# Kernel optimization log

Measured on AMD Instinct MI355X. Metric: run time of the kernel, lower is better.

## Reference

```python
import jax, jax.numpy as jnp
import numpy as np

EMBED_DIM = 1024
NUM_HEADS = 16
PROJ_DIM = EMBED_DIM // NUM_HEADS


def setup_inputs() -> dict:
    key = jax.random.key(0)
    ks = jax.random.split(key, 11)
    B, S, D = 2, 2048, EMBED_DIM
    scale = 1.0 / np.sqrt(D)
    inp = {
        'q': jax.random.normal(ks[0], (B, S, D), jnp.float32),
        'k': jax.random.normal(ks[1], (B, S, D), jnp.float32),
        'v': jax.random.normal(ks[2], (B, S, D), jnp.float32),
        'Wq': jax.random.normal(ks[3], (D, D), jnp.float32) * scale,
        'bq': jnp.zeros((D,), jnp.float32),
        'Wk': jax.random.normal(ks[4], (D, D), jnp.float32) * scale,
        'bk': jnp.zeros((D,), jnp.float32),
        'Wv': jax.random.normal(ks[5], (D, D), jnp.float32) * scale,
        'bv': jnp.zeros((D,), jnp.float32),
        'Wo': jax.random.normal(ks[6], (D, D), jnp.float32) * scale,
        'bo': jnp.zeros((D,), jnp.float32),
        'use_causal_mask': 1,
    }
    return inp


def _split_heads(x, B):
    # [B, S, D] -> [B, H, S, Pd]
    return x.reshape(B, -1, NUM_HEADS, PROJ_DIM).transpose(0, 2, 1, 3)


def reference(q, k, v, Wq, bq, Wk, bk, Wv, bv, Wo, bo, use_causal_mask):
    B, S, D = q.shape
    qh = _split_heads(q @ Wq + bq, B)
    kh = _split_heads(k @ Wk + bk, B)
    vh = _split_heads(v @ Wv + bv, B)
    # scaled dot-product attention; scores [B, H, S, S]
    logits = jnp.einsum('bhqd,bhkd->bhqk', qh, kh) / jnp.sqrt(
        jnp.asarray(PROJ_DIM, jnp.float32))
    if use_causal_mask:
        # faithful to source: logits += log(tril * 1e-9 + 1e-9)
        tril = jnp.tril(jnp.ones((S, S), dtype=logits.dtype))
        logits = logits + jnp.log(tril * 1e-9 + 1e-9)
    attn = jax.nn.softmax(logits, axis=-1)
    out = jnp.einsum('bhqk,bhkd->bhqd', attn, vh)
    out = out.transpose(0, 2, 1, 3).reshape(B, S, D)
    return out @ Wo + bo
```

## Files before the change

### kernel.cpp

```cpp
#include <hip/hip_runtime.h>
#include <hip/hip_bf16.h>
#include <stdint.h>

#define EMBED 1024
#define NH    16
#define PD    64
#define BATCH 2
#define SEQ   2048

typedef unsigned short u16;
typedef __attribute__((ext_vector_type(8))) short bf16x8;
typedef __attribute__((ext_vector_type(4))) float f32x4;

#define WAITALL() __builtin_amdgcn_s_waitcnt(0)

__device__ __forceinline__ float b2f(u16 x) {
  unsigned u = ((unsigned)x) << 16;
  return __builtin_bit_cast(float, u);
}
__device__ __forceinline__ u16 cvtb(float x) {
  __bf16 h = (__bf16)x;
  return __builtin_bit_cast(u16, h);
}
__device__ __forceinline__ float loadIn(const void* p, size_t i, int isf32) {
  return isf32 ? ((const float*)p)[i] : b2f(((const u16*)p)[i]);
}
__device__ __forceinline__ void async16(const void* g, void* l) {
  __builtin_amdgcn_global_load_lds((const __attribute__((address_space(1))) void*)g,
                                   (__attribute__((address_space(3))) void*)l,
                                   16, 0, 0);
}
__device__ __forceinline__ int detect_f32(const void* q) {
  unsigned w0 = ((const unsigned*)q)[threadIdx.x & 63];
  unsigned e = (w0 >> 7) & 0xffu;
  unsigned long long m = __ballot(e >= 110 && e <= 135);
  return (__popcll(m) < 32) ? 1 : 0;
}

__global__ __launch_bounds__(256) void conv_fused(
    const void* q, const void* k, const void* v,
    const void* Wq, const void* Wk, const void* Wv, const void* Wo,
    u16* qb, u16* kb, u16* vb, u16* WT_all) {
  __shared__ float sh[64][65];
  const int isf32 = detect_f32(q);

  if (blockIdx.y < 3) {
    size_t i = ((size_t)blockIdx.x * 256 + threadIdx.x) * 8;
    const void* src = (blockIdx.y == 0) ? q : (blockIdx.y == 1) ? k : v;
    u16* dst = (blockIdx.y == 0) ? qb : (blockIdx.y == 1) ? kb : vb;
    u16 tmp[8];
    if (isf32) {
      const float* s = (const float*)src + i;
      float4 a = *(const float4*)s;
      float4 b = *(const float4*)(s + 4);
      tmp[0] = cvtb(a.x); tmp[1] = cvtb(a.y); tmp[2] = cvtb(a.z); tmp[3] = cvtb(a.w);
      tmp[4] = cvtb(b.x); tmp[5] = cvtb(b.y); tmp[6] = cvtb(b.z); tmp[7] = cvtb(b.w);
    } else {
      const uint4 r = *(const uint4*)((const u16*)src + i);
      *(uint4*)tmp = r;
    }
    *(uint4*)(dst + i) = *(uint4*)tmp;
    return;
  }

  if (blockIdx.x >= 1024) return;
  const int z = blockIdx.x >> 8;
  const int xy = blockIdx.x & 255;
  const int bx = xy & 15, by = xy >> 4;
  const void* W = (z == 0) ? Wq : (z == 1) ? Wk : (z == 2) ? Wv : Wo;
  u16* WT = WT_all + (size_t)z * EMBED * EMBED;
  int r0 = by * 64, c0 = bx * 64;
  int col = threadIdx.x & 63;
  int rb  = threadIdx.x >> 6;
#pragma unroll
  for (int i = 0; i < 16; i++) {
    int row = i * 4 + rb;
    sh[row][col] = loadIn(W, (size_t)(r0 + row) * EMBED + c0 + col, isf32);
  }
  __syncthreads();
#pragma unroll
  for (int i = 0; i < 16; i++) {
    int row = i * 4 + rb;
    WT[(size_t)(c0 + row) * EMBED + r0 + col] = cvtb(sh[col][row]);
  }
}

__device__ __forceinline__ void gemm_stage(const u16* __restrict__ A,
                                           const u16* __restrict__ Bt,
                                           int tm, int tn, int kt,
                                           u16* As, u16* Bs, int tid) {
#pragma unroll
  for (int i = 0; i < 4; i++) {
    int c = i * 256 + tid;
    int row = c >> 3;
    int col = ((c & 7) << 3) ^ ((row & 7) << 3);
    async16(A + (size_t)(tm + row) * EMBED + kt + col, As + c * 8);
    async16(Bt + (size_t)(tn + row) * EMBED + kt + col, Bs + c * 8);
  }
}

__device__ __forceinline__ void gemm_compute(const u16* As, const u16* Bs,
                                             int wm, int wn, int l15, int quad,
                                             int rbx, f32x4 acc[4][4]) {
#pragma unroll
  for (int ks = 0; ks < 64; ks += 32) {
    int ko = (ks + quad * 8) ^ rbx;
    bf16x8 af[4], bf[4];
#pragma unroll
    for (int mt = 0; mt < 4; mt++)
      af[mt] = *(const bf16x8*)(As + (wm + mt * 16 + l15) * 64 + ko);
#pragma unroll
    for (int nt = 0; nt < 4; nt++)
      bf[nt] = *(const bf16x8*)(Bs + (wn + nt * 16 + l15) * 64 + ko);
#pragma unroll
    for (int mt = 0; mt < 4; mt++)
#pragma unroll
      for (int nt = 0; nt < 4; nt++)
        acc[mt][nt] = __builtin_amdgcn_mfma_f32_16x16x32_bf16(
            af[mt], bf[nt], acc[mt][nt], 0, 0, 0);
  }
}

__global__ __launch_bounds__(256) void qkv_gemm(
    const u16* qb, const u16* kb, const u16* vb, const u16* wts,
    const void* bq, const void* bk, const void* bv,
    u16* Qh, u16* Kh, u16* Vt, const void* qorig) {
  __shared__ __align__(16) u16 lds[2 * 128 * 64];
  const int isf32 = detect_f32(qorig);
  int z = blockIdx.z;
  const u16* A = (z == 0) ? qb : (z == 1) ? kb : vb;
  const u16* Bt = wts + (size_t)z * EMBED * EMBED;
  const void* bias = (z == 0) ? bq : (z == 1) ? bk : bv;
  int tm = blockIdx.y * 128, tn = blockIdx.x * 128;

  const int tid = threadIdx.x, lane = tid & 63, wv = tid >> 6;
  const int wm = (wv >> 1) * 64, wn = (wv & 1) * 64;
  const int l15 = lane & 15, quad = lane >> 4;
  const int rbx = (lane & 7) << 3;
  f32x4 acc[4][4];
  f32x4 zz = {0.f, 0.f, 0.f, 0.f};
#pragma unroll
  for (int i = 0; i < 4; i++)
#pragma unroll
    for (int j = 0; j < 4; j++) acc[i][j] = zz;

  for (int kt = 0; kt < EMBED; kt += 64) {
    gemm_stage(A, Bt, tm, tn, kt, lds, lds + 8192, tid);
    WAITALL();
    __syncthreads();
    gemm_compute(lds, lds + 8192, wm, wn, l15, quad, rbx, acc);
    __syncthreads();
  }

  int rbase = tm + wm + (quad << 2);
  int cbase = tn + wn + l15;
  if (z < 2) {
    u16* dst = (z == 0) ? Qh : Kh;
#pragma unroll
    for (int mt = 0; mt < 4; mt++)
#pragma unroll
      for (int nt = 0; nt < 4; nt++) {
        int col = cbase + nt * 16;
        float bv_ = loadIn(bias, col, isf32);
        int h = col >> 6, p = col & 63;
#pragma unroll
        for (int j = 0; j < 4; j++) {
          int row = rbase + mt * 16 + j;
          int b = row >> 11, s = row & 2047;
          dst[(((size_t)(b * NH + h) * SEQ) + s) * PD + p] =
              cvtb(acc[mt][nt][j] + bv_);
        }
      }
  } else {
#pragma unroll
    for (int mt = 0; mt < 4; mt++)
#pragma unroll
      for (int nt = 0; nt < 4; nt++) {
        int col = cbase + nt * 16;
        float bv_ = loadIn(bias, col, isf32);
        int h = col >> 6, p = col & 63;
        int row0 = rbase + mt * 16;
        int b = row0 >> 11, s0 = row0 & 2047;
        int beta = s0 >> 5, w = s0 & 31;
        int pos = (beta << 5) + (((w >> 2) & 3) << 3) + ((w >> 4) << 2);
        ushort4 pk;
        pk.x = cvtb(acc[mt][nt][0] + bv_);
        pk.y = cvtb(acc[mt][nt][1] + bv_);
        pk.z = cvtb(acc[mt][nt][2] + bv_);
        pk.w = cvtb(acc[mt][nt][3] + bv_);
        *(ushort4*)(Vt + ((size_t)(b * NH + h) * PD + p) * SEQ + pos) = pk;
      }
  }
}

__global__ __launch_bounds__(256, 4) void attn(const u16* __restrict__ Qh,
                                               const u16* __restrict__ Kh,
                                               const u16* __restrict__ Vt,
                                               u16* __restrict__ O,
                                               const int* __restrict__ maskflag) {
  __shared__ __align__(16) u16 sh[4 * 64 * 64];
  u16* const Ksb0 = sh;
  u16* const Ksb1 = sh + 4096;
  u16* const Vsb0 = sh + 8192;
  u16* const Vsb1 = sh + 12288;
  u16* const Qs   = Ksb1;

  const int lid = blockIdx.x + (blockIdx.y << 5);
  const int xcd = lid & 7, j = lid >> 3;
  const int bh = (xcd << 2) | (j & 3);
  const int qt = (j >> 2) * 64;

  const int tid = threadIdx.x, lane = tid & 63, wv = tid >> 6;
  const int l15 = lane & 15, quad = lane >> 4;
  const int rbx = (lane & 7) << 3;
  const size_t head = (size_t)bh * SEQ * PD;
  const bool causal = (maskflag[0] != 0);
  const float C = 0.18033688011112042f;

  const int c0 = tid, c1 = 256 + tid;
  const int r0 = c0 >> 3, r1 = c1 >> 3;
  const int x0 = ((c0 & 7) << 3) ^ ((r0 & 7) << 3);
  const int x1 = ((c1 & 7) << 3) ^ ((r1 & 7) << 3);

  async16(Qh + head + (size_t)(qt + r0) * PD + x0, Qs + c0 * 8);
  async16(Qh + head + (size_t)(qt + r1) * PD + x1, Qs + c1 * 8);
  async16(Kh + head + (size_t)r0 * PD + x0, Ksb0 + c0 * 8);
  async16(Kh + head + (size_t)r1 * PD + x1, Ksb0 + c1 * 8);
  async16(Vt + head + (size_t)r0 * SEQ + x0, Vsb0 + c0 * 8);
  async16(Vt + head + (size_t)r1 * SEQ + x1, Vsb0 + c1 * 8);
  WAITALL();
  __syncthreads();

  bf16x8 qf[2];
#pragma unroll
  for (int ks = 0; ks < 2; ks++) {
    int ko = (ks * 32 + quad * 8) ^ rbx;
    qf[ks] = *(const bf16x8*)(Qs + (wv * 16 + l15) * 64 + ko);
  }
  __syncthreads();

  float lacc = 0.f;
  f32x4 oacc[4];
  f32x4 z4 = {0.f, 0.f, 0.f, 0.f};
#pragma unroll
  for (int mt = 0; mt < 4; mt++) oacc[mt] = z4;

  const int rowq = qt + wv * 16;
  const int qrow = rowq + l15;

  for (int t = 0; t < SEQ / 64; t++) {
    const int k0 = t * 64;
    const int cur = t & 1;
    if (t + 1 < SEQ / 64) {
      const int kn = k0 + 64;
      u16* Kn = cur ? Ksb0 : Ksb1;
      u16* Vn = cur ? Vsb0 : Vsb1;
      async16(Kh + head + (size_t)(kn + r0) * PD + x0, Kn + c0 * 8);
      async16(Kh + head + (size_t)(kn + r1) * PD + x1, Kn + c1 * 8);
      async16(Vt + head + (size_t)r0 * SEQ + kn + x0, Vn + c0 * 8);
      async16(Vt + head + (size_t)r1 * SEQ + kn + x1, Vn + c1 * 8);
    }
    const u16* Ksc = cur ? Ksb1 : Ksb0;
    const u16* Vsc = cur ? Vsb1 : Vsb0;

    f32x4 st[4];
#pragma unroll
    for (int kt = 0; kt < 4; kt++) st[kt] = z4;
    __builtin_amdgcn_s_setprio(1);
#pragma unroll
    for (int ks = 0; ks < 2; ks++) {
      int ko = (ks * 32 + quad * 8) ^ rbx;
#pragma unroll
      for (int kt = 0; kt < 4; kt++) {
        bf16x8 kf = *(const bf16x8*)(Ksc + (kt * 16 + l15) * 64 + ko);
        st[kt] = __builtin_amdgcn_mfma_f32_16x16x32_bf16(kf, qf[ks], st[kt], 0, 0, 0);
      }
    }
    __builtin_amdgcn_s_setprio(0);

    const int mode = !causal ? 0 : (k0 > qt + 63 ? 2 : (k0 + 63 <= qt ? 0 : 1));
    const float ub = (mode == 2) ? -17.f : -16.f;
    unsigned pw[2][4];
#pragma unroll
    for (int kt = 0; kt < 4; kt++) {
      float p[4];
#pragma unroll
      for (int r = 0; r < 4; r++) {
        float bias = ub;
        if (mode == 1) {
          int kappa = k0 + kt * 16 + 4 * quad + r;
          bias = (kappa > qrow) ? -17.f : -16.f;
        }
        p[r] = exp2f(fmaf(st[kt][r], C, bias));
      }
      lacc += (p[0] + p[1]) + (p[2] + p[3]);
      pw[kt >> 1][(kt & 1) * 2 + 0] =
          (unsigned)cvtb(p[0]) | ((unsigned)cvtb(p[1]) << 16);
      pw[kt >> 1][(kt & 1) * 2 + 1] =
          (unsigned)cvtb(p[2]) | ((unsigned)cvtb(p[3]) << 16);
    }

    __builtin_amdgcn_s_setprio(1);
#pragma unroll
    for (int p = 0; p < 2; p++) {
      bf16x8 pf = __builtin_bit_cast(bf16x8,
          (uint4){pw[p][0], pw[p][1], pw[p][2], pw[p][3]});
#pragma unroll
      for (int mt = 0; mt < 4; mt++) {
        int row = mt * 16 + l15;
        int chunk = ((p << 2) + quad) ^ (row & 7);
        bf16x8 vf = *(const bf16x8*)(Vsc + row * 64 + (chunk << 3));
        oacc[mt] = __builtin_amdgcn_mfma_f32_16x16x32_bf16(vf, pf, oacc[mt], 0, 0, 0);
      }
    }
    __builtin_amdgcn_s_setprio(0);
    WAITALL();
    __syncthreads();
  }

  lacc += __shfl_xor(lacc, 16, 64);
  lacc += __shfl_xor(lacc, 32, 64);
  float inv = 1.f / lacc;

  const int b = bh >> 4, h = bh & 15;
#pragma unroll
  for (int mt = 0; mt < 4; mt++) {
    ushort4 w;
    w.x = cvtb(oacc[mt][0] * inv);
    w.y = cvtb(oacc[mt][1] * inv);
    w.z = cvtb(oacc[mt][2] * inv);
    w.w = cvtb(oacc[mt][3] * inv);
    *(ushort4*)(O + ((size_t)b * SEQ + qrow) * EMBED + h * PD + mt * 16 +
                4 * quad) = w;
  }
}

__global__ __launch_bounds__(256) void out_gemm(const u16* __restrict__ Ob,
                                                const u16* __restrict__ WoT,
                                                const void* __restrict__ bo,
                                                void* __restrict__ out,
                                                const void* __restrict__ qorig) {
  __shared__ __align__(16) u16 lds[4 * 128 * 64];
  const int isf32 = detect_f32(qorig);
  int tm = blockIdx.y * 128, tn = blockIdx.x * 128;
  const int tid = threadIdx.x, lane = tid & 63, wv = tid >> 6;
  const int wm = (wv >> 1) * 64, wn = (wv & 1) * 64;
  const int l15 = lane & 15, quad = lane >> 4;
  const int rbx = (lane & 7) << 3;
  f32x4 acc[4][4];
  f32x4 zz = {0.f, 0.f, 0.f, 0.f};
#pragma unroll
  for (int i = 0; i < 4; i++)
#pragma unroll
    for (int j = 0; j < 4; j++) acc[i][j] = zz;

  gemm_stage(Ob, WoT, tm, tn, 0, lds, lds + 8192, tid);
  WAITALL();
  __syncthreads();
  for (int kt = 0; kt < EMBED; kt += 64) {
    const int cur = (kt >> 6) & 1;
    u16* curb = lds + cur * 16384;
    if (kt + 64 < EMBED)
      gemm_stage(Ob, WoT, tm, tn, kt + 64, lds + (cur ^ 1) * 16384,
                 lds + (cur ^ 1) * 16384 + 8192, tid);
    gemm_compute(curb, curb + 8192, wm, wn, l15, quad, rbx, acc);
    WAITALL();
    __syncthreads();
  }

  int rbase = tm + wm + (quad << 2);
  int cbase = tn + wn + l15;
#pragma unroll
  for (int mt = 0; mt < 4; mt++)
#pragma unroll
    for (int nt = 0; nt < 4; nt++) {
      int col = cbase + nt * 16;
      float bv_ = loadIn(bo, col, isf32);
#pragma unroll
      for (int j = 0; j < 4; j++) {
        int row = rbase + mt * 16 + j;
        float val = acc[mt][nt][j] + bv_;
        size_t off = (size_t)row * EMBED + col;
        if (isf32) ((float*)out)[off] = val;
        else       ((u16*)out)[off]   = cvtb(val);
      }
    }
}

extern "C" void kernel_launch(void* const* d_in, const int* in_sizes, int n_in,
                              void* d_out, int out_size, void* d_ws, size_t ws_size,
                              hipStream_t stream) {
  const void* q  = d_in[0];
  const void* k  = d_in[1];
  const void* v  = d_in[2];
  const void* Wq = d_in[3];
  const void* bq = d_in[4];
  const void* Wk = d_in[5];
  const void* bk = d_in[6];
  const void* Wv = d_in[7];
  const void* bv = d_in[8];
  const void* Wo = d_in[9];
  const void* bo = d_in[10];
  const int* msk = (const int*)d_in[11];

  char* ws = (char*)d_ws;
  u16*  qb    = (u16*)(ws + 64);
  u16*  kb    = qb + (size_t)4194304;
  u16*  vb    = kb + (size_t)4194304;
  u16*  WT    = vb + (size_t)4194304;
  u16*  Qh    = WT + (size_t)4194304;
  u16*  Kh    = Qh + (size_t)4194304;
  u16*  Vt    = Kh + (size_t)4194304;
  u16*  Ob    = Vt + (size_t)4194304;

  conv_fused<<<dim3(2048, 4), 256, 0, stream>>>(q, k, v, Wq, Wk, Wv, Wo,
                                                qb, kb, vb, WT);
  qkv_gemm<<<dim3(8, 32, 3), 256, 0, stream>>>(qb, kb, vb, WT, bq, bk, bv,
                                               Qh, Kh, Vt, q);
  attn<<<dim3(32, 32), 256, 0, stream>>>(Qh, Kh, Vt, Ob, msk);
  out_gemm<<<dim3(8, 32), 256, 0, stream>>>(Ob, WT + (size_t)3 * 1048576,
                                            bo, d_out, q);
}
```

Before: 276.2 us.

## Double-buffer QKV GEMM and split attention waves over query and key halves

The QKV projection GEMM now double-buffers its LDS tiles, prefetching the next K-slice while computing the current one. This removes one barrier per iteration and overlaps global loads with MFMA work. The attention kernel changes from each wave owning 16 query rows across all 64 keys to a 2x2 split: each wave owns 32 query rows and 32 keys, so K and V fragments loaded from LDS are reused across two query tiles. Partial outputs and row sums from the two key halves are combined at the end through LDS, which adds a reduction step and more accumulator registers.

```diff
diff --git a/kernel.cpp b/kernel.cpp
--- a/kernel.cpp
+++ b/kernel.cpp
@@ -125,7 +125,7 @@
     const u16* qb, const u16* kb, const u16* vb, const u16* wts,
     const void* bq, const void* bk, const void* bv,
     u16* Qh, u16* Kh, u16* Vt, const void* qorig) {
-  __shared__ __align__(16) u16 lds[2 * 128 * 64];
+  __shared__ __align__(16) u16 lds[4 * 128 * 64];
   const int isf32 = detect_f32(qorig);
   int z = blockIdx.z;
   const u16* A = (z == 0) ? qb : (z == 1) ? kb : vb;
@@ -144,11 +144,17 @@
 #pragma unroll
     for (int j = 0; j < 4; j++) acc[i][j] = zz;
 
+  gemm_stage(A, Bt, tm, tn, 0, lds, lds + 8192, tid);
+  WAITALL();
+  __syncthreads();
   for (int kt = 0; kt < EMBED; kt += 64) {
-    gemm_stage(A, Bt, tm, tn, kt, lds, lds + 8192, tid);
+    const int cur = (kt >> 6) & 1;
+    u16* curb = lds + cur * 16384;
+    if (kt + 64 < EMBED)
+      gemm_stage(A, Bt, tm, tn, kt + 64, lds + (cur ^ 1) * 16384,
+                 lds + (cur ^ 1) * 16384 + 8192, tid);
+    gemm_compute(curb, curb + 8192, wm, wn, l15, quad, rbx, acc);
     WAITALL();
-    __syncthreads();
-    gemm_compute(lds, lds + 8192, wm, wn, l15, quad, rbx, acc);
     __syncthreads();
   }
 
@@ -211,6 +217,8 @@
   const int qt = (j >> 2) * 64;
 
   const int tid = threadIdx.x, lane = tid & 63, wv = tid >> 6;
+  const int qh = wv & 1;
+  const int kh = wv >> 1;
   const int l15 = lane & 15, quad = lane >> 4;
   const int rbx = (lane & 7) << 3;
   const size_t head = (size_t)bh * SEQ * PD;
@@ -231,22 +239,24 @@
   WAITALL();
   __syncthreads();
 
-  bf16x8 qf[2];
+  bf16x8 qf[2][2];
 #pragma unroll
   for (int ks = 0; ks < 2; ks++) {
     int ko = (ks * 32 + quad * 8) ^ rbx;
-    qf[ks] = *(const bf16x8*)(Qs + (wv * 16 + l15) * 64 + ko);
-  }
-  __syncthreads();
-
-  float lacc = 0.f;
-  f32x4 oacc[4];
+    qf[ks][0] = *(const bf16x8*)(Qs + (qh * 32 + l15) * 64 + ko);
+    qf[ks][1] = *(const bf16x8*)(Qs + (qh * 32 + 16 + l15) * 64 + ko);
+  }
+  __syncthreads();
+
+  float lacc[2] = {0.f, 0.f};
+  f32x4 oacc[4][2];
   f32x4 z4 = {0.f, 0.f, 0.f, 0.f};
 #pragma unroll
-  for (int mt = 0; mt < 4; mt++) oacc[mt] = z4;
-
-  const int rowq = qt + wv * 16;
-  const int qrow = rowq + l15;
+  for (int mt = 0; mt < 4; mt++)
+#pragma unroll
+    for (int qx = 0; qx < 2; qx++) oacc[mt][qx] = z4;
+
+  const int qrow0 = qt + qh * 32 + l15;
 
   for (int t = 0; t < SEQ / 64; t++) {
     const int k0 = t * 64;
@@ -263,17 +273,20 @@
     const u16* Ksc = cur ? Ksb1 : Ksb0;
     const u16* Vsc = cur ? Vsb1 : Vsb0;
 
-    f32x4 st[4];
-#pragma unroll
-    for (int kt = 0; kt < 4; kt++) st[kt] = z4;
+    f32x4 st[2][2];
+#pragma unroll
+    for (int kx = 0; kx < 2; kx++)
+#pragma unroll
+      for (int qx = 0; qx < 2; qx++) st[kx][qx] = z4;
     __builtin_amdgcn_s_setprio(1);
 #pragma unroll
     for (int ks = 0; ks < 2; ks++) {
       int ko = (ks * 32 + quad * 8) ^ rbx;
 #pragma unroll
-      for (int kt = 0; kt < 4; kt++) {
-        bf16x8 kf = *(const bf16x8*)(Ksc + (kt * 16 + l15) * 64 + ko);
-        st[kt] = __builtin_amdgcn_mfma_f32_16x16x32_bf16(kf, qf[ks], st[kt], 0, 0, 0);
+      for (int kx = 0; kx < 2; kx++) {
+        bf16x8 kf = *(const bf16x8*)(Ksc + (kh * 32 + kx * 16 + l15) * 64 + ko);
+        st[kx][0] = __builtin_amdgcn_mfma_f32_16x16x32_bf16(kf, qf[ks][0], st[kx][0], 0, 0, 0);
+        st[kx][1] = __builtin_amdgcn_mfma_f32_16x16x32_bf16(kf, qf[ks][1], st[kx][1], 0, 0, 0);
       }
     }
     __builtin_amdgcn_s_setprio(0);
@@ -282,56 +295,85 @@
     const float ub = (mode == 2) ? -17.f : -16.f;
     unsigned pw[2][4];
 #pragma unroll
-    for (int kt = 0; kt < 4; kt++) {
-      float p[4];
-#pragma unroll
-      for (int r = 0; r < 4; r++) {
-        float bias = ub;
-        if (mode == 1) {
-          int kappa = k0 + kt * 16 + 4 * quad + r;
-          bias = (kappa > qrow) ? -17.f : -16.f;
+    for (int kx = 0; kx < 2; kx++) {
+#pragma unroll
+      for (int qx = 0; qx < 2; qx++) {
+        const int qrow = qrow0 + qx * 16;
+        float p[4];
+#pragma unroll
+        for (int r = 0; r < 4; r++) {
+          float bias = ub;
+          if (mode == 1) {
+            int kappa = k0 + kh * 32 + kx * 16 + 4 * quad + r;
+            bias = (kappa > qrow) ? -17.f : -16.f;
+          }
+          p[r] = exp2f(fmaf(st[kx][qx][r], C, bias));
         }
-        p[r] = exp2f(fmaf(st[kt][r], C, bias));
-      }
-      lacc += (p[0] + p[1]) + (p[2] + p[3]);
-      pw[kt >> 1][(kt & 1) * 2 + 0] =
-          (unsigned)cvtb(p[0]) | ((unsigned)cvtb(p[1]) << 16);
-      pw[kt >> 1][(kt & 1) * 2 + 1] =
-          (unsigned)cvtb(p[2]) | ((unsigned)cvtb(p[3]) << 16);
+        lacc[qx] += (p[0] + p[1]) + (p[2] + p[3]);
+        pw[qx][kx * 2 + 0] =
+            (unsigned)cvtb(p[0]) | ((unsigned)cvtb(p[1]) << 16);
+        pw[qx][kx * 2 + 1] =
+            (unsigned)cvtb(p[2]) | ((unsigned)cvtb(p[3]) << 16);
+      }
     }
 
     __builtin_amdgcn_s_setprio(1);
-#pragma unroll
-    for (int p = 0; p < 2; p++) {
-      bf16x8 pf = __builtin_bit_cast(bf16x8,
-          (uint4){pw[p][0], pw[p][1], pw[p][2], pw[p][3]});
-#pragma unroll
-      for (int mt = 0; mt < 4; mt++) {
-        int row = mt * 16 + l15;
-        int chunk = ((p << 2) + quad) ^ (row & 7);
-        bf16x8 vf = *(const bf16x8*)(Vsc + row * 64 + (chunk << 3));
-        oacc[mt] = __builtin_amdgcn_mfma_f32_16x16x32_bf16(vf, pf, oacc[mt], 0, 0, 0);
-      }
+    bf16x8 pf0 = __builtin_bit_cast(bf16x8,
+        (uint4){pw[0][0], pw[0][1], pw[0][2], pw[0][3]});
+    bf16x8 pf1 = __builtin_bit_cast(bf16x8,
+        (uint4){pw[1][0], pw[1][1], pw[1][2], pw[1][3]});
+#pragma unroll
+    for (int mt = 0; mt < 4; mt++) {
+      int row = mt * 16 + l15;
+      int chunk = ((kh << 2) + quad) ^ (row & 7);
+      bf16x8 vf = *(const bf16x8*)(Vsc + row * 64 + (chunk << 3));
+      oacc[mt][0] = __builtin_amdgcn_mfma_f32_16x16x32_bf16(vf, pf0, oacc[mt][0], 0, 0, 0);
+      oacc[mt][1] = __builtin_amdgcn_mfma_f32_16x16x32_bf16(vf, pf1, oacc[mt][1], 0, 0, 0);
     }
     __builtin_amdgcn_s_setprio(0);
     WAITALL();
     __syncthreads();
   }
 
-  lacc += __shfl_xor(lacc, 16, 64);
-  lacc += __shfl_xor(lacc, 32, 64);
-  float inv = 1.f / lacc;
-
-  const int b = bh >> 4, h = bh & 15;
-#pragma unroll
-  for (int mt = 0; mt < 4; mt++) {
-    ushort4 w;
-    w.x = cvtb(oacc[mt][0] * inv);
-    w.y = cvtb(oacc[mt][1] * inv);
-    w.z = cvtb(oacc[mt][2] * inv);
-    w.w = cvtb(oacc[mt][3] * inv);
-    *(ushort4*)(O + ((size_t)b * SEQ + qrow) * EMBED + h * PD + mt * 16 +
-                4 * quad) = w;
+#pragma unroll
+  for (int qx = 0; qx < 2; qx++) {
+    lacc[qx] += __shfl_xor(lacc[qx], 16, 64);
+    lacc[qx] += __shfl_xor(lacc[qx], 32, 64);
+  }
+
+  float* red = (float*)sh;
+  if (kh == 1) {
+#pragma unroll
+    for (int mt = 0; mt < 4; mt++)
+#pragma unroll
+      for (int qx = 0; qx < 2; qx++)
+        *(f32x4*)(red + qh * 2048 + (mt * 2 + qx) * 256 + lane * 4) =
+            oacc[mt][qx];
+    red[4096 + qh * 128 + lane] = lacc[0];
+    red[4096 + qh * 128 + 64 + lane] = lacc[1];
+  }
+  __syncthreads();
+  if (kh == 0) {
+    float l0 = lacc[0] + red[4096 + qh * 128 + lane];
+    float l1 = lacc[1] + red[4096 + qh * 128 + 64 + lane];
+    float inv[2] = {1.f / l0, 1.f / l1};
+    const int b = bh >> 4, h = bh & 15;
+#pragma unroll
+    for (int mt = 0; mt < 4; mt++) {
+#pragma unroll
+      for (int qx = 0; qx < 2; qx++) {
+        f32x4 o = oacc[mt][qx] +
+                  *(const f32x4*)(red + qh * 2048 + (mt * 2 + qx) * 256 + lane * 4);
+        int qrow = qrow0 + qx * 16;
+        ushort4 w;
+        w.x = cvtb(o[0] * inv[qx]);
+        w.y = cvtb(o[1] * inv[qx]);
+        w.z = cvtb(o[2] * inv[qx]);
+        w.w = cvtb(o[3] * inv[qx]);
+        *(ushort4*)(O + ((size_t)b * SEQ + qrow) * EMBED + h * PD + mt * 16 +
+                    4 * quad) = w;
+      }
+    }
   }
 }
 
```

Result: no change. 275.4 us (-0.3%).
